# Optimization experiments

Measured on AMD Instinct MI355X. Metric: run time of the kernel, lower is better.

## Reference

```python
import jax, jax.numpy as jnp
import numpy as np

N_HEADS = 16
NEG = -1000000000.0  # masked_fill value from the original code


def setup_inputs() -> dict:
    key = jax.random.key(0)
    ks = jax.random.split(key, 7)
    D = 1024
    x = jax.random.normal(ks[0], (2, 2048, D), dtype=jnp.float32)
    s = 1.0 / np.sqrt(D)
    Wq = jax.random.normal(ks[1], (D, D), dtype=jnp.float32) * s
    bq = jax.random.normal(ks[2], (D,), dtype=jnp.float32) * 0.01
    Wk = jax.random.normal(ks[3], (D, D), dtype=jnp.float32) * s
    bk = jax.random.normal(ks[4], (D,), dtype=jnp.float32) * 0.01
    Wv = jax.random.normal(ks[5], (D, D), dtype=jnp.float32) * s
    bv = jax.random.normal(ks[6], (D,), dtype=jnp.float32) * 0.01
    return {"x": x, "Wq": Wq, "bq": bq, "Wk": Wk, "bk": bk, "Wv": Wv, "bv": bv}


def reference(x, Wq, bq, Wk, bk, Wv, bv):
    B, S, D = x.shape
    H = N_HEADS
    dh = D // H
    # nn.Linear: x @ W.T + b
    Q = (x @ Wq.T + bq).reshape(B, S, H, dh)
    K = (x @ Wk.T + bk).reshape(B, S, H, dh)
    V = (x @ Wv.T + bv).reshape(B, S, H, dh)
    # NOTE: original scales by sqrt(n_heads), not sqrt(d_head) -- faithful.
    scale = jnp.asarray(H, x.dtype) ** 0.5
    scores = jnp.einsum('bqhd,bkhd->bhqk', Q, K) / scale  # [B,H,S,S]
    # Original: mask = triu(ones, diag=1); scores.masked_fill(mask == 0, -1e9)
    # i.e. positions where the STRICT-UPPER mask is False (lower triangle incl.
    # diagonal) get -1e9. Faithful reproduction of that (buggy) behavior.
    triu = jnp.triu(jnp.ones((S, S), dtype=bool), k=1)  # [S,S]
    scores = jnp.where(triu[None, None, :, :], scores, jnp.asarray(NEG, x.dtype))
    probs = jax.nn.softmax(scores, axis=-1)
    # dropout is identity at inference
    out = jnp.einsum('bhqk,bkhd->bqhd', probs, V).reshape(B, S, D)
    return out
```

## Files before the change

### kernel.cpp

```cpp
#include <hip/hip_runtime.h>
#include <stdint.h>

typedef unsigned short u16;
typedef __attribute__((ext_vector_type(8))) short bf16x8;
typedef __attribute__((ext_vector_type(4))) float floatx4;

#define MFMA16(a, b, c) __builtin_amdgcn_mfma_f32_16x16x32_bf16(a, b, c, 0, 0, 0)
#define MEMFENCE asm volatile("" ::: "memory")

#if __has_builtin(__builtin_amdgcn_exp2f)
#define EXP2(x) __builtin_amdgcn_exp2f(x)
#else
#define EXP2(x) __expf(0.6931471805599453f * (x))
#endif

__device__ __forceinline__ u16 f2bf(float f) {
  unsigned u = __builtin_bit_cast(unsigned, f);
  return (u16)((u + 0x7FFFu + ((u >> 16) & 1u)) >> 16);
}
__device__ __forceinline__ u16 f2bf_hu(float f) {
  return (u16)((__builtin_bit_cast(unsigned, f) + 0x8000u) >> 16);
}
__device__ __forceinline__ float bf2f(u16 v) {
  return __builtin_bit_cast(float, (unsigned)v << 16);
}

__device__ __forceinline__ void glds16(void* lds, const void* g) {
  __builtin_amdgcn_global_load_lds((const __attribute__((address_space(1))) void*)g,
                                   (__attribute__((address_space(3))) void*)lds,
                                   16, 0, 0);
}

__global__ __launch_bounds__(256) void cvt_all(
    const float* __restrict__ x, const float* __restrict__ w0,
    const float* __restrict__ w1, const float* __restrict__ w2,
    u16* __restrict__ xb, u16* __restrict__ Wb) {
  const int bid = blockIdx.x;
  const float* src;
  u16* dst;
  int i;
  if (bid < 4096) {
    src = x; dst = xb; i = bid * 256 + threadIdx.x;
  } else {
    const int z = (bid - 4096) >> 10;
    src = (z == 0) ? w0 : (z == 1) ? w1 : w2;
    dst = Wb + (size_t)z * (1024 * 1024);
    i = ((bid - 4096) & 1023) * 256 + threadIdx.x;
  }
  float4 f = reinterpret_cast<const float4*>(src)[i];
  ushort4 o;
  o.x = f2bf(f.x); o.y = f2bf(f.y); o.z = f2bf(f.z); o.w = f2bf(f.w);
  reinterpret_cast<ushort4*>(dst)[i] = o;
}

__global__ __launch_bounds__(256, 3) void qkv_gemm(
    const u16* __restrict__ xb, const u16* __restrict__ Wb,
    const float* __restrict__ bq, const float* __restrict__ bk,
    const float* __restrict__ bv,
    u16* __restrict__ Qb, u16* __restrict__ Kb, u16* __restrict__ VTb) {
  __shared__ __attribute__((aligned(16))) u16 smem[2 * 128 * 64];
  u16* As = smem;
  u16* Bs = smem + 128 * 64;

  const int tid = threadIdx.x;
  const int w = tid >> 6, lane = tid & 63;
  const int lo = lane & 15, quad = lane >> 4;
  const int which = blockIdx.z;
  const int m0 = blockIdx.x * 128, n0 = blockIdx.y * 128;

  const u16* W = Wb + (size_t)which * (1024 * 1024);
  const int wm = (w >> 1) * 64, wn = (w & 1) * 64;

  floatx4 acc[4][4];
  for (int i = 0; i < 4; ++i)
    for (int j = 0; j < 4; ++j) acc[i][j] = (floatx4)0.f;

  const int arow = lane >> 3;
  const int aswz = ((lane & 7) ^ arow) * 8;

  for (int kt = 0; kt < 16; ++kt) {
    const int k0 = kt * 64;
    for (int j = 0; j < 4; ++j) {
      const int seg = w * 4 + j;
      glds16(As + seg * 512, xb + (size_t)(m0 + seg * 8 + arow) * 1024 + k0 + aswz);
      glds16(Bs + seg * 512, W + (size_t)(n0 + seg * 8 + arow) * 1024 + k0 + aswz);
    }
    __syncthreads();
    for (int kk = 0; kk < 2; ++kk) {
      const int swz = ((kk * 4 + quad) ^ (lo & 7)) * 8;
      bf16x8 af[4], bfr[4];
      for (int it = 0; it < 4; ++it)
        af[it] = *reinterpret_cast<const bf16x8*>(As + (wm + it * 16 + lo) * 64 + swz);
      for (int jt = 0; jt < 4; ++jt)
        bfr[jt] = *reinterpret_cast<const bf16x8*>(Bs + (wn + jt * 16 + lo) * 64 + swz);
      for (int it = 0; it < 4; ++it)
        for (int jt = 0; jt < 4; ++jt)
          acc[it][jt] = MFMA16(af[it], bfr[jt], acc[it][jt]);
    }
    __syncthreads();
  }

  const float* bias = (which == 0) ? bq : (which == 1) ? bk : bv;
  float bb[4];
  for (int jt = 0; jt < 4; ++jt) bb[jt] = bias[n0 + wn + jt * 16 + lo];
  const int b = m0 >> 11;

  if (which < 2) {
    const float scl = (which == 0) ? 0.36067376022224085f : 1.0f;
    u16* Tw = smem + w * (16 * 72);
    const int hblk = (n0 + wn) >> 6;
    u16* dst = ((which == 0) ? Qb : Kb) +
               ((size_t)(b * 16 + hblk) * 2048 + ((m0 & 2047) + wm)) * 64;
    for (int it = 0; it < 4; ++it) {
      for (int jt = 0; jt < 4; ++jt)
        for (int r = 0; r < 4; ++r) {
          const int m = quad * 4 + r, col = jt * 16 + lo;
          Tw[m * 72 + (((col >> 3) ^ (m & 7)) * 8) + (col & 7)] =
              f2bf((acc[it][jt][r] + bb[jt]) * scl);
        }
      MEMFENCE;
      for (int rd = 0; rd < 2; ++rd) {
        const int sr = rd * 8 + (lane >> 3), d8 = lane & 7;
        bf16x8 v = *reinterpret_cast<const bf16x8*>(Tw + sr * 72 + ((d8 ^ (sr & 7)) * 8));
        *reinterpret_cast<bf16x8*>(dst + (size_t)(it * 16 + sr) * 64 + d8 * 8) = v;
      }
      MEMFENCE;
    }
  } else {
    for (int pass = 0; pass < 2; ++pass) {
      if ((wm >> 6) == pass) {
        for (int it = 0; it < 4; ++it)
          for (int jt = 0; jt < 4; ++jt)
            for (int r = 0; r < 4; ++r) {
              const int n = wn + jt * 16 + lo;
              const int m = it * 16 + quad * 4 + r;
              smem[n * 72 + (((m >> 3) ^ (n & 7)) * 8) + (m & 7)] =
                  f2bf(acc[it][jt][r] + bb[jt]);
            }
      }
      __syncthreads();
      for (int rd = 0; rd < 4; ++rd) {
        const int n = (tid >> 3) + rd * 32, m8 = tid & 7;
        bf16x8 v = *reinterpret_cast<const bf16x8*>(smem + n * 72 + ((m8 ^ (n & 7)) * 8));
        const int ng = n0 + n, h = ng >> 6, d = ng & 63;
        const int s = (m0 & 2047) + pass * 64 + m8 * 8;
        *reinterpret_cast<bf16x8*>(VTb + ((size_t)(b * 16 + h) * 64 + d) * 2048 + s) = v;
      }
      __syncthreads();
    }
  }
}

__global__ __launch_bounds__(128, 2) void attn(
    const u16* __restrict__ Qb, const u16* __restrict__ Kb,
    const u16* __restrict__ VTb, float* __restrict__ out) {
  __shared__ __attribute__((aligned(16))) u16 Ks[2][64 * 64];
  __shared__ __attribute__((aligned(16))) u16 Vs[2][64 * 64];
  __shared__ __attribute__((aligned(16))) u16 Pt[2][2][16 * 64];

  const int L = blockIdx.x;
  const int bh = L & 31;
  const int p = L >> 5;

  const int tid = threadIdx.x, w = tid >> 6, lane = tid & 63;
  const int lo = lane & 15, quad = lane >> 4;

  const u16* Qh = Qb + (size_t)bh * (2048 * 64);
  const u16* Kh = Kb + (size_t)bh * (2048 * 64);
  const u16* Vh = VTb + (size_t)bh * (64 * 2048);

  const int srow8 = lane >> 3, sblk = lane & 7;
  const int sswz = (sblk ^ srow8) * 8;

  const int b = bh >> 4, hh = bh & 15;

  for (int half = 0; half < 2; ++half) {
    const int item = half ? (31 - p) : p;
    const int kstart = item;

    int qrow[2];
    bf16x8 qf[2][2];
    for (int s = 0; s < 2; ++s) {
      qrow[s] = item * 64 + w * 32 + s * 16 + lo;
      qf[s][0] = *reinterpret_cast<const bf16x8*>(Qh + (size_t)qrow[s] * 64 + quad * 8);
      qf[s][1] = *reinterpret_cast<const bf16x8*>(Qh + (size_t)qrow[s] * 64 + 32 + quad * 8);
    }

    float lrun[2] = {0.f, 0.f};
    floatx4 acc[2][4];
    for (int s = 0; s < 2; ++s)
      for (int dt = 0; dt < 4; ++dt) acc[s][dt] = (floatx4)0.f;

    for (int j = 0; j < 4; ++j) {
      const int b8 = (w * 4 + j) * 8;
      glds16(&Ks[0][b8 * 64], Kh + (size_t)(kstart * 64 + b8 + srow8) * 64 + sswz);
      glds16(&Vs[0][b8 * 64], Vh + (size_t)(b8 + srow8) * 2048 + kstart * 64 + sswz);
    }
    __syncthreads();

    for (int kt = kstart; kt < 32; ++kt) {
      const int cur = (kt - kstart) & 1, nxt = cur ^ 1;
      if (kt < 31)
        for (int j = 0; j < 4; ++j) {
          const int b8 = (w * 4 + j) * 8;
          glds16(&Ks[nxt][b8 * 64], Kh + (size_t)((kt + 1) * 64 + b8 + srow8) * 64 + sswz);
          glds16(&Vs[nxt][b8 * 64], Vh + (size_t)(b8 + srow8) * 2048 + (kt + 1) * 64 + sswz);
        }
      const u16* ksb = Ks[cur];
      const u16* vsb = Vs[cur];

      const bool maskp = (kt == kstart);

      floatx4 sc[2][4];
      for (int s = 0; s < 2; ++s)
        for (int t = 0; t < 4; ++t) sc[s][t] = (floatx4)0.f;
      for (int kk = 0; kk < 2; ++kk) {
        const int swz = ((kk * 4 + quad) ^ (lo & 7)) * 8;
        for (int t = 0; t < 4; ++t) {
          bf16x8 ka = *reinterpret_cast<const bf16x8*>(ksb + (t * 16 + lo) * 64 + swz);
          sc[0][t] = MFMA16(ka, qf[0][kk], sc[0][t]);
          sc[1][t] = MFMA16(ka, qf[1][kk], sc[1][t]);
        }
      }

      for (int s = 0; s < 2; ++s) {
        u16* ptw = &Pt[w][s][0];
        for (int t = 0; t < 4; ++t) {
          float p0 = EXP2(sc[s][t][0]), p1 = EXP2(sc[s][t][1]);
          float p2 = EXP2(sc[s][t][2]), p3 = EXP2(sc[s][t][3]);
          if (maskp) {
            const int key = kt * 64 + t * 16 + quad * 4;
            p0 = (key + 0 > qrow[s]) ? p0 : 0.f;
            p1 = (key + 1 > qrow[s]) ? p1 : 0.f;
            p2 = (key + 2 > qrow[s]) ? p2 : 0.f;
            p3 = (key + 3 > qrow[s]) ? p3 : 0.f;
          }
          lrun[s] += (p0 + p1) + (p2 + p3);
          ushort4 pk;
          pk.x = f2bf_hu(p0); pk.y = f2bf_hu(p1);
          pk.z = f2bf_hu(p2); pk.w = f2bf_hu(p3);
          u16* pdst = ptw + lo * 64 +
                      (((2 * t + (quad >> 1)) ^ (lo & 7)) * 8) + (quad & 1) * 4;
          *reinterpret_cast<ushort4*>(pdst) = pk;
        }
      }
      MEMFENCE;

      for (int kk = 0; kk < 2; ++kk) {
        const int pswz = ((kk * 4 + quad) ^ (lo & 7)) * 8;
        bf16x8 pb0 = *reinterpret_cast<const bf16x8*>(&Pt[w][0][lo * 64] + pswz);
        bf16x8 pb1 = *reinterpret_cast<const bf16x8*>(&Pt[w][1][lo * 64] + pswz);
        for (int dt = 0; dt < 4; ++dt) {
          bf16x8 va = *reinterpret_cast<const bf16x8*>(
              vsb + (dt * 16 + lo) * 64 + pswz);
          acc[0][dt] = MFMA16(va, pb0, acc[0][dt]);
          acc[1][dt] = MFMA16(va, pb1, acc[1][dt]);
        }
      }
      MEMFENCE;
      __syncthreads();
    }

    for (int s = 0; s < 2; ++s) {
      float l = lrun[s];
      l += __shfl_xor(l, 16);
      l += __shfl_xor(l, 32);
      if (l != 0.f) {
        const float rl = 1.f / l;
        float* op = out + ((size_t)(b * 2048 + qrow[s])) * 1024 + hh * 64 + quad * 4;
        for (int dt = 0; dt < 4; ++dt) {
          float4 o4;
          o4.x = acc[s][dt][0] * rl; o4.y = acc[s][dt][1] * rl;
          o4.z = acc[s][dt][2] * rl; o4.w = acc[s][dt][3] * rl;
          *reinterpret_cast<float4*>(op + dt * 16) = o4;
        }
      }
    }
  }
}

__global__ __launch_bounds__(256) void fix2047(const u16* __restrict__ VTb,
                                               float* __restrict__ out) {
  const int bh = blockIdx.x;
  const u16* Vh = VTb + (size_t)bh * (64 * 2048);
  const int t = threadIdx.x;
  const int d = t >> 2, j = t & 3;
  float s = 0.f;
  const u16* row = Vh + (size_t)d * 2048 + j * 512;
  for (int i = 0; i < 64; ++i) {
    bf16x8 v = *reinterpret_cast<const bf16x8*>(row + i * 8);
    for (int e = 0; e < 8; ++e) s += bf2f((u16)v[e]);
  }
  s += __shfl_xor(s, 1);
  s += __shfl_xor(s, 2);
  if (j == 0) {
    const int b = bh >> 4, h = bh & 15;
    out[((size_t)(b * 2048 + 2047)) * 1024 + h * 64 + d] = s * (1.f / 2048.f);
  }
}

extern "C" void kernel_launch(void* const* d_in, const int* in_sizes, int n_in,
                              void* d_out, int out_size, void* d_ws, size_t ws_size,
                              hipStream_t stream) {
  const float* x  = (const float*)d_in[0];
  const float* Wq = (const float*)d_in[1];
  const float* bq = (const float*)d_in[2];
  const float* Wk = (const float*)d_in[3];
  const float* bk = (const float*)d_in[4];
  const float* Wv = (const float*)d_in[5];
  const float* bv = (const float*)d_in[6];
  float* out = (float*)d_out;

  char* ws = (char*)d_ws;
  u16* xb  = (u16*)(ws);
  u16* Wb  = (u16*)(ws + (8u << 20));
  u16* Qb  = (u16*)(ws + (14u << 20));
  u16* Kb  = (u16*)(ws + (22u << 20));
  u16* VTb = (u16*)(ws + (30u << 20));

  cvt_all<<<7168, 256, 0, stream>>>(x, Wq, Wk, Wv, xb, Wb);
  qkv_gemm<<<dim3(32, 8, 3), 256, 0, stream>>>(xb, Wb, bq, bk, bv, Qb, Kb, VTb);
  attn<<<dim3(512), 128, 0, stream>>>(Qb, Kb, VTb, out);
  fix2047<<<dim3(32), 256, 0, stream>>>(VTb, out);
}
```

Baseline: 169.5 us.

## Split attention work into one query tile per block with four waves

The attention kernel previously used 512 blocks of two waves, each handling a pair of query tiles (p and 31-p) with 32 rows per wave. It now launches 1024 blocks of four waves, each block owning one 64-row query tile with 16 rows per wave. Tiles are assigned in a zigzag order across block indices to spread the causal-style load imbalance. This raises parallelism and occupancy, and lets four waves share each K/V tile loaded into shared memory. The cost is that each wave issues fewer MFMAs per K/V fragment read, and the per-block load is no longer balanced by pairing tiles.

```diff
diff --git a/kernel.cpp b/kernel.cpp
--- a/kernel.cpp
+++ b/kernel.cpp
@@ -151,16 +151,19 @@
   }
 }
 
-__global__ __launch_bounds__(128, 2) void attn(
+__global__ __launch_bounds__(256, 4) void attn(
     const u16* __restrict__ Qb, const u16* __restrict__ Kb,
     const u16* __restrict__ VTb, float* __restrict__ out) {
   __shared__ __attribute__((aligned(16))) u16 Ks[2][64 * 64];
   __shared__ __attribute__((aligned(16))) u16 Vs[2][64 * 64];
-  __shared__ __attribute__((aligned(16))) u16 Pt[2][2][16 * 64];
+  __shared__ __attribute__((aligned(16))) u16 Pt[4][16 * 64];
 
   const int L = blockIdx.x;
   const int bh = L & 31;
-  const int p = L >> 5;
+  const int j = L >> 5;
+  const int g = j >> 3, r = j & 7;
+  const int qi = (g == 0) ? r : (g == 1) ? 15 - r : (g == 2) ? 16 + r : 31 - r;
+  const int kstart = qi;
 
   const int tid = threadIdx.x, w = tid >> 6, lane = tid & 63;
   const int lo = lane & 15, quad = lane >> 4;
@@ -169,112 +172,93 @@
   const u16* Kh = Kb + (size_t)bh * (2048 * 64);
   const u16* Vh = VTb + (size_t)bh * (64 * 2048);
 
+  const int qrow = qi * 64 + w * 16 + lo;
+  bf16x8 qf[2];
+  qf[0] = *reinterpret_cast<const bf16x8*>(Qh + (size_t)qrow * 64 + quad * 8);
+  qf[1] = *reinterpret_cast<const bf16x8*>(Qh + (size_t)qrow * 64 + 32 + quad * 8);
+
+  float lrun = 0.f;
+  floatx4 acc[4];
+  for (int dt = 0; dt < 4; ++dt) acc[dt] = (floatx4)0.f;
+
   const int srow8 = lane >> 3, sblk = lane & 7;
   const int sswz = (sblk ^ srow8) * 8;
 
+  for (int jj = 0; jj < 2; ++jj) {
+    const int b8 = (w * 2 + jj) * 8;
+    glds16(&Ks[0][b8 * 64], Kh + (size_t)(kstart * 64 + b8 + srow8) * 64 + sswz);
+    glds16(&Vs[0][b8 * 64], Vh + (size_t)(b8 + srow8) * 2048 + kstart * 64 + sswz);
+  }
+  __syncthreads();
+
+  for (int kt = kstart; kt < 32; ++kt) {
+    const int cur = (kt - kstart) & 1, nxt = cur ^ 1;
+    if (kt < 31)
+      for (int jj = 0; jj < 2; ++jj) {
+        const int b8 = (w * 2 + jj) * 8;
+        glds16(&Ks[nxt][b8 * 64], Kh + (size_t)((kt + 1) * 64 + b8 + srow8) * 64 + sswz);
+        glds16(&Vs[nxt][b8 * 64], Vh + (size_t)(b8 + srow8) * 2048 + (kt + 1) * 64 + sswz);
+      }
+    const u16* ksb = Ks[cur];
+    const u16* vsb = Vs[cur];
+
+    const bool maskp = (kt == kstart);
+
+    floatx4 sc[4];
+    for (int t = 0; t < 4; ++t) sc[t] = (floatx4)0.f;
+    for (int kk = 0; kk < 2; ++kk) {
+      const int swz = ((kk * 4 + quad) ^ (lo & 7)) * 8;
+      for (int t = 0; t < 4; ++t) {
+        bf16x8 ka = *reinterpret_cast<const bf16x8*>(ksb + (t * 16 + lo) * 64 + swz);
+        sc[t] = MFMA16(ka, qf[kk], sc[t]);
+      }
+    }
+
+    u16* ptw = &Pt[w][0];
+    for (int t = 0; t < 4; ++t) {
+      float p0 = EXP2(sc[t][0]), p1 = EXP2(sc[t][1]);
+      float p2 = EXP2(sc[t][2]), p3 = EXP2(sc[t][3]);
+      if (maskp) {
+        const int key = kt * 64 + t * 16 + quad * 4;
+        p0 = (key + 0 > qrow) ? p0 : 0.f;
+        p1 = (key + 1 > qrow) ? p1 : 0.f;
+        p2 = (key + 2 > qrow) ? p2 : 0.f;
+        p3 = (key + 3 > qrow) ? p3 : 0.f;
+      }
+      lrun += (p0 + p1) + (p2 + p3);
+      ushort4 pk;
+      pk.x = f2bf_hu(p0); pk.y = f2bf_hu(p1);
+      pk.z = f2bf_hu(p2); pk.w = f2bf_hu(p3);
+      u16* pdst = ptw + lo * 64 +
+                  (((2 * t + (quad >> 1)) ^ (lo & 7)) * 8) + (quad & 1) * 4;
+      *reinterpret_cast<ushort4*>(pdst) = pk;
+    }
+    MEMFENCE;
+
+    for (int kk = 0; kk < 2; ++kk) {
+      const int pswz = ((kk * 4 + quad) ^ (lo & 7)) * 8;
+      bf16x8 pb = *reinterpret_cast<const bf16x8*>(ptw + lo * 64 + pswz);
+      for (int dt = 0; dt < 4; ++dt) {
+        bf16x8 va = *reinterpret_cast<const bf16x8*>(vsb + (dt * 16 + lo) * 64 + pswz);
+        acc[dt] = MFMA16(va, pb, acc[dt]);
+      }
+    }
+    MEMFENCE;
+    __syncthreads();
+  }
+
   const int b = bh >> 4, hh = bh & 15;
-
-  for (int half = 0; half < 2; ++half) {
-    const int item = half ? (31 - p) : p;
-    const int kstart = item;
-
-    int qrow[2];
-    bf16x8 qf[2][2];
-    for (int s = 0; s < 2; ++s) {
-      qrow[s] = item * 64 + w * 32 + s * 16 + lo;
-      qf[s][0] = *reinterpret_cast<const bf16x8*>(Qh + (size_t)qrow[s] * 64 + quad * 8);
-      qf[s][1] = *reinterpret_cast<const bf16x8*>(Qh + (size_t)qrow[s] * 64 + 32 + quad * 8);
-    }
-
-    float lrun[2] = {0.f, 0.f};
-    floatx4 acc[2][4];
-    for (int s = 0; s < 2; ++s)
-      for (int dt = 0; dt < 4; ++dt) acc[s][dt] = (floatx4)0.f;
-
-    for (int j = 0; j < 4; ++j) {
-      const int b8 = (w * 4 + j) * 8;
-      glds16(&Ks[0][b8 * 64], Kh + (size_t)(kstart * 64 + b8 + srow8) * 64 + sswz);
-      glds16(&Vs[0][b8 * 64], Vh + (size_t)(b8 + srow8) * 2048 + kstart * 64 + sswz);
-    }
-    __syncthreads();
-
-    for (int kt = kstart; kt < 32; ++kt) {
-      const int cur = (kt - kstart) & 1, nxt = cur ^ 1;
-      if (kt < 31)
-        for (int j = 0; j < 4; ++j) {
-          const int b8 = (w * 4 + j) * 8;
-          glds16(&Ks[nxt][b8 * 64], Kh + (size_t)((kt + 1) * 64 + b8 + srow8) * 64 + sswz);
-          glds16(&Vs[nxt][b8 * 64], Vh + (size_t)(b8 + srow8) * 2048 + (kt + 1) * 64 + sswz);
-        }
-      const u16* ksb = Ks[cur];
-      const u16* vsb = Vs[cur];
-
-      const bool maskp = (kt == kstart);
-
-      floatx4 sc[2][4];
-      for (int s = 0; s < 2; ++s)
-        for (int t = 0; t < 4; ++t) sc[s][t] = (floatx4)0.f;
-      for (int kk = 0; kk < 2; ++kk) {
-        const int swz = ((kk * 4 + quad) ^ (lo & 7)) * 8;
-        for (int t = 0; t < 4; ++t) {
-          bf16x8 ka = *reinterpret_cast<const bf16x8*>(ksb + (t * 16 + lo) * 64 + swz);
-          sc[0][t] = MFMA16(ka, qf[0][kk], sc[0][t]);
-          sc[1][t] = MFMA16(ka, qf[1][kk], sc[1][t]);
-        }
-      }
-
-      for (int s = 0; s < 2; ++s) {
-        u16* ptw = &Pt[w][s][0];
-        for (int t = 0; t < 4; ++t) {
-          float p0 = EXP2(sc[s][t][0]), p1 = EXP2(sc[s][t][1]);
-          float p2 = EXP2(sc[s][t][2]), p3 = EXP2(sc[s][t][3]);
-          if (maskp) {
-            const int key = kt * 64 + t * 16 + quad * 4;
-            p0 = (key + 0 > qrow[s]) ? p0 : 0.f;
-            p1 = (key + 1 > qrow[s]) ? p1 : 0.f;
-            p2 = (key + 2 > qrow[s]) ? p2 : 0.f;
-            p3 = (key + 3 > qrow[s]) ? p3 : 0.f;
-          }
-          lrun[s] += (p0 + p1) + (p2 + p3);
-          ushort4 pk;
-          pk.x = f2bf_hu(p0); pk.y = f2bf_hu(p1);
-          pk.z = f2bf_hu(p2); pk.w = f2bf_hu(p3);
-          u16* pdst = ptw + lo * 64 +
-                      (((2 * t + (quad >> 1)) ^ (lo & 7)) * 8) + (quad & 1) * 4;
-          *reinterpret_cast<ushort4*>(pdst) = pk;
-        }
-      }
-      MEMFENCE;
-
-      for (int kk = 0; kk < 2; ++kk) {
-        const int pswz = ((kk * 4 + quad) ^ (lo & 7)) * 8;
-        bf16x8 pb0 = *reinterpret_cast<const bf16x8*>(&Pt[w][0][lo * 64] + pswz);
-        bf16x8 pb1 = *reinterpret_cast<const bf16x8*>(&Pt[w][1][lo * 64] + pswz);
-        for (int dt = 0; dt < 4; ++dt) {
-          bf16x8 va = *reinterpret_cast<const bf16x8*>(
-              vsb + (dt * 16 + lo) * 64 + pswz);
-          acc[0][dt] = MFMA16(va, pb0, acc[0][dt]);
-          acc[1][dt] = MFMA16(va, pb1, acc[1][dt]);
-        }
-      }
-      MEMFENCE;
-      __syncthreads();
-    }
-
-    for (int s = 0; s < 2; ++s) {
-      float l = lrun[s];
-      l += __shfl_xor(l, 16);
-      l += __shfl_xor(l, 32);
-      if (l != 0.f) {
-        const float rl = 1.f / l;
-        float* op = out + ((size_t)(b * 2048 + qrow[s])) * 1024 + hh * 64 + quad * 4;
-        for (int dt = 0; dt < 4; ++dt) {
-          float4 o4;
-          o4.x = acc[s][dt][0] * rl; o4.y = acc[s][dt][1] * rl;
-          o4.z = acc[s][dt][2] * rl; o4.w = acc[s][dt][3] * rl;
-          *reinterpret_cast<float4*>(op + dt * 16) = o4;
-        }
-      }
+  float l = lrun;
+  l += __shfl_xor(l, 16);
+  l += __shfl_xor(l, 32);
+  if (l != 0.f) {
+    const float rl = 1.f / l;
+    float* op = out + ((size_t)(b * 2048 + qrow)) * 1024 + hh * 64 + quad * 4;
+    for (int dt = 0; dt < 4; ++dt) {
+      float4 o4;
+      o4.x = acc[dt][0] * rl; o4.y = acc[dt][1] * rl;
+      o4.z = acc[dt][2] * rl; o4.w = acc[dt][3] * rl;
+      *reinterpret_cast<float4*>(op + dt * 16) = o4;
     }
   }
 }
@@ -320,6 +304,6 @@
 
   cvt_all<<<7168, 256, 0, stream>>>(x, Wq, Wk, Wv, xb, Wb);
   qkv_gemm<<<dim3(32, 8, 3), 256, 0, stream>>>(xb, Wb, bq, bk, bv, Qb, Kb, VTb);
-  attn<<<dim3(512), 128, 0, stream>>>(Qb, Kb, VTb, out);
+  attn<<<dim3(1024), 256, 0, stream>>>(Qb, Kb, VTb, out);
   fix2047<<<dim3(32), 256, 0, stream>>>(VTb, out);
 }
```

Result: faster. 151.5 us (-10.6%).

## Keep P in registers via permlane swaps, fold fix2047 into attn, reschedule tiles

Applied to the files above, without the earlier changes.

The softmax probabilities are now packed with v_cvt_pk_bf16_f32 and rearranged into the MFMA B-operand layout using permlane32/16 swaps, so the LDS round-trip through the Pt buffer goes away. The separate fix2047 kernel becomes 32 extra blocks at the front of the attention grid, which saves a launch. Each block now handles one query tile instead of a pair (1056 blocks), and a grouped ordering is meant to balance the causal work. This adds more blocks with less work each and relies on gfx950-specific permlane instructions.

```diff
diff --git a/kernel.cpp b/kernel.cpp
--- a/kernel.cpp
+++ b/kernel.cpp
@@ -18,11 +18,20 @@
   unsigned u = __builtin_bit_cast(unsigned, f);
   return (u16)((u + 0x7FFFu + ((u >> 16) & 1u)) >> 16);
 }
-__device__ __forceinline__ u16 f2bf_hu(float f) {
-  return (u16)((__builtin_bit_cast(unsigned, f) + 0x8000u) >> 16);
-}
 __device__ __forceinline__ float bf2f(u16 v) {
   return __builtin_bit_cast(float, (unsigned)v << 16);
+}
+
+__device__ __forceinline__ unsigned cvtpk(float lo, float hi) {
+  unsigned d;
+  asm("v_cvt_pk_bf16_f32 %0, %1, %2" : "=v"(d) : "v"(lo), "v"(hi));
+  return d;
+}
+__device__ __forceinline__ void perm32swap(unsigned& a, unsigned& b) {
+  asm("v_permlane32_swap_b32 %0, %1" : "+v"(a), "+v"(b));
+}
+__device__ __forceinline__ void perm16swap(unsigned& a, unsigned& b) {
+  asm("v_permlane16_swap_b32 %0, %1" : "+v"(a), "+v"(b));
 }
 
 __device__ __forceinline__ void glds16(void* lds, const void* g) {
@@ -156,11 +165,33 @@
     const u16* __restrict__ VTb, float* __restrict__ out) {
   __shared__ __attribute__((aligned(16))) u16 Ks[2][64 * 64];
   __shared__ __attribute__((aligned(16))) u16 Vs[2][64 * 64];
-  __shared__ __attribute__((aligned(16))) u16 Pt[2][2][16 * 64];
 
   const int L = blockIdx.x;
-  const int bh = L & 31;
-  const int p = L >> 5;
+  if (L < 32) {
+    const int bh = L;
+    const u16* Vh = VTb + (size_t)bh * (64 * 2048);
+    const int t = threadIdx.x;
+    const int d = t >> 1, jj = t & 1;
+    float s = 0.f;
+    const u16* row = Vh + (size_t)d * 2048 + jj * 1024;
+    for (int i = 0; i < 128; ++i) {
+      bf16x8 v = *reinterpret_cast<const bf16x8*>(row + i * 8);
+      for (int e = 0; e < 8; ++e) s += bf2f((u16)v[e]);
+    }
+    s += __shfl_xor(s, 1);
+    if (jj == 0) {
+      const int b = bh >> 4, h = bh & 15;
+      out[((size_t)(b * 2048 + 2047)) * 1024 + h * 64 + d] = s * (1.f / 2048.f);
+    }
+    return;
+  }
+
+  const int M = L - 32;
+  const int bh = M & 31;
+  const int j = M >> 5;
+  const int g = j >> 3, r = j & 7;
+  const int qi = (g == 0) ? r : (g == 1) ? 15 - r : (g == 2) ? 16 + r : 31 - r;
+  const int kstart = qi;
 
   const int tid = threadIdx.x, w = tid >> 6, lane = tid & 63;
   const int lo = lane & 15, quad = lane >> 4;
@@ -169,133 +200,120 @@
   const u16* Kh = Kb + (size_t)bh * (2048 * 64);
   const u16* Vh = VTb + (size_t)bh * (64 * 2048);
 
+  int qrow[2];
+  bf16x8 qf[2][2];
+#pragma unroll
+  for (int s = 0; s < 2; ++s) {
+    qrow[s] = qi * 64 + w * 32 + s * 16 + lo;
+    qf[s][0] = *reinterpret_cast<const bf16x8*>(Qh + (size_t)qrow[s] * 64 + quad * 8);
+    qf[s][1] = *reinterpret_cast<const bf16x8*>(Qh + (size_t)qrow[s] * 64 + 32 + quad * 8);
+  }
+
+  float lrun[2] = {0.f, 0.f};
+  floatx4 acc[2][4];
+#pragma unroll
+  for (int s = 0; s < 2; ++s)
+#pragma unroll
+    for (int dt = 0; dt < 4; ++dt) acc[s][dt] = (floatx4)0.f;
+
   const int srow8 = lane >> 3, sblk = lane & 7;
   const int sswz = (sblk ^ srow8) * 8;
 
+#pragma unroll
+  for (int jj = 0; jj < 4; ++jj) {
+    const int b8 = (w * 4 + jj) * 8;
+    glds16(&Ks[0][b8 * 64], Kh + (size_t)(kstart * 64 + b8 + srow8) * 64 + sswz);
+    glds16(&Vs[0][b8 * 64], Vh + (size_t)(b8 + srow8) * 2048 + kstart * 64 + sswz);
+  }
+  __syncthreads();
+
+  for (int kt = kstart; kt < 32; ++kt) {
+    const int cur = (kt - kstart) & 1, nxt = cur ^ 1;
+    if (kt < 31)
+#pragma unroll
+      for (int jj = 0; jj < 4; ++jj) {
+        const int b8 = (w * 4 + jj) * 8;
+        glds16(&Ks[nxt][b8 * 64], Kh + (size_t)((kt + 1) * 64 + b8 + srow8) * 64 + sswz);
+        glds16(&Vs[nxt][b8 * 64], Vh + (size_t)(b8 + srow8) * 2048 + (kt + 1) * 64 + sswz);
+      }
+    const u16* ksb = Ks[cur];
+    const u16* vsb = Vs[cur];
+
+    const bool maskp = (kt == kstart);
+
+    floatx4 sc[2][4];
+#pragma unroll
+    for (int s = 0; s < 2; ++s)
+#pragma unroll
+      for (int t = 0; t < 4; ++t) sc[s][t] = (floatx4)0.f;
+#pragma unroll
+    for (int kk = 0; kk < 2; ++kk) {
+      const int swz = ((kk * 4 + quad) ^ (lo & 7)) * 8;
+#pragma unroll
+      for (int t = 0; t < 4; ++t) {
+        bf16x8 ka = *reinterpret_cast<const bf16x8*>(ksb + (t * 16 + lo) * 64 + swz);
+        sc[0][t] = MFMA16(ka, qf[0][kk], sc[0][t]);
+        sc[1][t] = MFMA16(ka, qf[1][kk], sc[1][t]);
+      }
+    }
+
+    unsigned pkA[2][4], pkB[2][4];
+#pragma unroll
+    for (int s = 0; s < 2; ++s)
+#pragma unroll
+      for (int t = 0; t < 4; ++t) {
+        float p0 = EXP2(sc[s][t][0]), p1 = EXP2(sc[s][t][1]);
+        float p2 = EXP2(sc[s][t][2]), p3 = EXP2(sc[s][t][3]);
+        if (maskp) {
+          const int key = kt * 64 + t * 16 + quad * 4;
+          p0 = (key + 0 > qrow[s]) ? p0 : 0.f;
+          p1 = (key + 1 > qrow[s]) ? p1 : 0.f;
+          p2 = (key + 2 > qrow[s]) ? p2 : 0.f;
+          p3 = (key + 3 > qrow[s]) ? p3 : 0.f;
+        }
+        lrun[s] += (p0 + p1) + (p2 + p3);
+        pkA[s][t] = cvtpk(p0, p1);
+        pkB[s][t] = cvtpk(p2, p3);
+      }
+
+#pragma unroll
+    for (int s = 0; s < 2; ++s) {
+#pragma unroll
+      for (int kk = 0; kk < 2; ++kk) {
+        unsigned a0 = pkA[s][2 * kk], a1 = pkA[s][2 * kk + 1];
+        unsigned b0 = pkB[s][2 * kk], b1 = pkB[s][2 * kk + 1];
+        perm32swap(a0, a1); perm16swap(a0, a1);
+        perm32swap(b0, b1); perm16swap(b0, b1);
+        uint4 pw; pw.x = a0; pw.y = b0; pw.z = a1; pw.w = b1;
+        const bf16x8 pb = __builtin_bit_cast(bf16x8, pw);
+        const int pswz = ((kk * 4 + quad) ^ (lo & 7)) * 8;
+#pragma unroll
+        for (int dt = 0; dt < 4; ++dt) {
+          bf16x8 va = *reinterpret_cast<const bf16x8*>(vsb + (dt * 16 + lo) * 64 + pswz);
+          acc[s][dt] = MFMA16(va, pb, acc[s][dt]);
+        }
+      }
+    }
+    __syncthreads();
+  }
+
   const int b = bh >> 4, hh = bh & 15;
-
-  for (int half = 0; half < 2; ++half) {
-    const int item = half ? (31 - p) : p;
-    const int kstart = item;
-
-    int qrow[2];
-    bf16x8 qf[2][2];
-    for (int s = 0; s < 2; ++s) {
-      qrow[s] = item * 64 + w * 32 + s * 16 + lo;
-      qf[s][0] = *reinterpret_cast<const bf16x8*>(Qh + (size_t)qrow[s] * 64 + quad * 8);
-      qf[s][1] = *reinterpret_cast<const bf16x8*>(Qh + (size_t)qrow[s] * 64 + 32 + quad * 8);
-    }
-
-    float lrun[2] = {0.f, 0.f};
-    floatx4 acc[2][4];
-    for (int s = 0; s < 2; ++s)
-      for (int dt = 0; dt < 4; ++dt) acc[s][dt] = (floatx4)0.f;
-
-    for (int j = 0; j < 4; ++j) {
-      const int b8 = (w * 4 + j) * 8;
-      glds16(&Ks[0][b8 * 64], Kh + (size_t)(kstart * 64 + b8 + srow8) * 64 + sswz);
-      glds16(&Vs[0][b8 * 64], Vh + (size_t)(b8 + srow8) * 2048 + kstart * 64 + sswz);
-    }
-    __syncthreads();
-
-    for (int kt = kstart; kt < 32; ++kt) {
-      const int cur = (kt - kstart) & 1, nxt = cur ^ 1;
-      if (kt < 31)
-        for (int j = 0; j < 4; ++j) {
-          const int b8 = (w * 4 + j) * 8;
-          glds16(&Ks[nxt][b8 * 64], Kh + (size_t)((kt + 1) * 64 + b8 + srow8) * 64 + sswz);
-          glds16(&Vs[nxt][b8 * 64], Vh + (size_t)(b8 + srow8) * 2048 + (kt + 1) * 64 + sswz);
-        }
-      const u16* ksb = Ks[cur];
-      const u16* vsb = Vs[cur];
-
-      const bool maskp = (kt == kstart);
-
-      floatx4 sc[2][4];
-      for (int s = 0; s < 2; ++s)
-        for (int t = 0; t < 4; ++t) sc[s][t] = (floatx4)0.f;
-      for (int kk = 0; kk < 2; ++kk) {
-        const int swz = ((kk * 4 + quad) ^ (lo & 7)) * 8;
-        for (int t = 0; t < 4; ++t) {
-          bf16x8 ka = *reinterpret_cast<const bf16x8*>(ksb + (t * 16 + lo) * 64 + swz);
-          sc[0][t] = MFMA16(ka, qf[0][kk], sc[0][t]);
-          sc[1][t] = MFMA16(ka, qf[1][kk], sc[1][t]);
-        }
-      }
-
-      for (int s = 0; s < 2; ++s) {
-        u16* ptw = &Pt[w][s][0];
-        for (int t = 0; t < 4; ++t) {
-          float p0 = EXP2(sc[s][t][0]), p1 = EXP2(sc[s][t][1]);
-          float p2 = EXP2(sc[s][t][2]), p3 = EXP2(sc[s][t][3]);
-          if (maskp) {
-            const int key = kt * 64 + t * 16 + quad * 4;
-            p0 = (key + 0 > qrow[s]) ? p0 : 0.f;
-            p1 = (key + 1 > qrow[s]) ? p1 : 0.f;
-            p2 = (key + 2 > qrow[s]) ? p2 : 0.f;
-            p3 = (key + 3 > qrow[s]) ? p3 : 0.f;
-          }
-          lrun[s] += (p0 + p1) + (p2 + p3);
-          ushort4 pk;
-          pk.x = f2bf_hu(p0); pk.y = f2bf_hu(p1);
-          pk.z = f2bf_hu(p2); pk.w = f2bf_hu(p3);
-          u16* pdst = ptw + lo * 64 +
-                      (((2 * t + (quad >> 1)) ^ (lo & 7)) * 8) + (quad & 1) * 4;
-          *reinterpret_cast<ushort4*>(pdst) = pk;
-        }
-      }
-      MEMFENCE;
-
-      for (int kk = 0; kk < 2; ++kk) {
-        const int pswz = ((kk * 4 + quad) ^ (lo & 7)) * 8;
-        bf16x8 pb0 = *reinterpret_cast<const bf16x8*>(&Pt[w][0][lo * 64] + pswz);
-        bf16x8 pb1 = *reinterpret_cast<const bf16x8*>(&Pt[w][1][lo * 64] + pswz);
-        for (int dt = 0; dt < 4; ++dt) {
-          bf16x8 va = *reinterpret_cast<const bf16x8*>(
-              vsb + (dt * 16 + lo) * 64 + pswz);
-          acc[0][dt] = MFMA16(va, pb0, acc[0][dt]);
-          acc[1][dt] = MFMA16(va, pb1, acc[1][dt]);
-        }
-      }
-      MEMFENCE;
-      __syncthreads();
-    }
-
-    for (int s = 0; s < 2; ++s) {
-      float l = lrun[s];
-      l += __shfl_xor(l, 16);
-      l += __shfl_xor(l, 32);
-      if (l != 0.f) {
-        const float rl = 1.f / l;
-        float* op = out + ((size_t)(b * 2048 + qrow[s])) * 1024 + hh * 64 + quad * 4;
-        for (int dt = 0; dt < 4; ++dt) {
-          float4 o4;
-          o4.x = acc[s][dt][0] * rl; o4.y = acc[s][dt][1] * rl;
-          o4.z = acc[s][dt][2] * rl; o4.w = acc[s][dt][3] * rl;
-          *reinterpret_cast<float4*>(op + dt * 16) = o4;
-        }
-      }
-    }
-  }
-}
-
-__global__ __launch_bounds__(256) void fix2047(const u16* __restrict__ VTb,
-                                               float* __restrict__ out) {
-  const int bh = blockIdx.x;
-  const u16* Vh = VTb + (size_t)bh * (64 * 2048);
-  const int t = threadIdx.x;
-  const int d = t >> 2, j = t & 3;
-  float s = 0.f;
-  const u16* row = Vh + (size_t)d * 2048 + j * 512;
-  for (int i = 0; i < 64; ++i) {
-    bf16x8 v = *reinterpret_cast<const bf16x8*>(row + i * 8);
-    for (int e = 0; e < 8; ++e) s += bf2f((u16)v[e]);
-  }
-  s += __shfl_xor(s, 1);
-  s += __shfl_xor(s, 2);
-  if (j == 0) {
-    const int b = bh >> 4, h = bh & 15;
-    out[((size_t)(b * 2048 + 2047)) * 1024 + h * 64 + d] = s * (1.f / 2048.f);
+#pragma unroll
+  for (int s = 0; s < 2; ++s) {
+    float l = lrun[s];
+    l += __shfl_xor(l, 16);
+    l += __shfl_xor(l, 32);
+    if (l != 0.f) {
+      const float rl = 1.f / l;
+      float* op = out + ((size_t)(b * 2048 + qrow[s])) * 1024 + hh * 64 + quad * 4;
+#pragma unroll
+      for (int dt = 0; dt < 4; ++dt) {
+        float4 o4;
+        o4.x = acc[s][dt][0] * rl; o4.y = acc[s][dt][1] * rl;
+        o4.z = acc[s][dt][2] * rl; o4.w = acc[s][dt][3] * rl;
+        *reinterpret_cast<float4*>(op + dt * 16) = o4;
+      }
+    }
   }
 }
 
@@ -320,6 +338,5 @@
 
   cvt_all<<<7168, 256, 0, stream>>>(x, Wq, Wk, Wv, xb, Wb);
   qkv_gemm<<<dim3(32, 8, 3), 256, 0, stream>>>(xb, Wb, bq, bk, bv, Qb, Kb, VTb);
-  attn<<<dim3(512), 128, 0, stream>>>(Qb, Kb, VTb, out);
-  fix2047<<<dim3(32), 256, 0, stream>>>(VTb, out);
-}
+  attn<<<dim3(1056), 128, 0, stream>>>(Qb, Kb, VTb, out);
+}
```

After: 148.8 us. 1.14x faster.
